# Kernel optimization log

Hardware: AMD Instinct MI355X
Metric: run time of the kernel (lower is better)

The kernel has to match this reference:

```python
import jax, jax.numpy as jnp
import numpy as np

B, N, C = 4, 1024, 23          # batch, nodes, scalar input channels (Rs_in=[(23,0)])
NB, H = 3, 100                 # cosine basis size, radial MLP hidden width
MAX_R = 3.0                    # CosineBasisModel max_radius
D1, D2, D3 = 30, 10, 1         # fc1/fc2/fc3 head dims


def setup_inputs() -> dict:
    key = jax.random.key(0)
    ks = jax.random.split(key, 12)
    features = jax.random.normal(ks[0], (B, N, C), jnp.float32)
    # random points inside a box comparable to max_radius so edges hit the basis support
    geometry = jax.random.uniform(ks[1], (B, N, 3), jnp.float32) * MAX_R
    # radial MLP (CosineBasisModel): NB -> H (relu) -> C weights (l=0 -> l=0 path, mul 23*1)
    W_rb1 = jax.random.normal(ks[2], (NB, H), jnp.float32) / np.sqrt(NB)
    b_rb1 = jnp.zeros((H,), jnp.float32)
    W_rb2 = jax.random.normal(ks[3], (H, C), jnp.float32) / np.sqrt(H)
    b_rb2 = jnp.zeros((C,), jnp.float32)
    # dense MLP head: Linear(N,30) -> Linear(30,10) -> Linear(10,1)
    W_fc1 = jax.random.normal(ks[4], (N, D1), jnp.float32) / np.sqrt(N)
    b_fc1 = jnp.zeros((D1,), jnp.float32)
    W_fc2 = jax.random.normal(ks[5], (D1, D2), jnp.float32) / np.sqrt(D1)
    b_fc2 = jnp.zeros((D2,), jnp.float32)
    W_fc3 = jax.random.normal(ks[6], (D2, D3), jnp.float32) / np.sqrt(D2)
    b_fc3 = jnp.zeros((D3,), jnp.float32)
    return {
        "features": features, "geometry": geometry,
        "W_rb1": W_rb1, "b_rb1": b_rb1, "W_rb2": W_rb2, "b_rb2": b_rb2,
        "W_fc1": W_fc1, "b_fc1": b_fc1, "W_fc2": W_fc2, "b_fc2": b_fc2,
        "W_fc3": W_fc3, "b_fc3": b_fc3,
    }


def _cosine_basis(r):
    """e3nn CosineBasisModel basis: cos^2 bumps centered on linspace(0,max_r,NB). r: [...]->[...,NB]."""
    radii = jnp.linspace(0.0, MAX_R, NB, dtype=r.dtype)
    step = radii[1] - radii[0]
    u = (r[..., None] - radii) / step
    half_pi = jnp.asarray(np.pi / 2, r.dtype)
    return jnp.where(jnp.abs(u) < 1.0, jnp.cos(half_pi * u) ** 2, jnp.zeros_like(u))


def reference(features, geometry, W_rb1, b_rb1, W_rb2, b_rb2,
              W_fc1, b_fc1, W_fc2, b_fc2, W_fc3, b_fc3):
    diff = geometry[:, :, None, :] - geometry[:, None, :, :]      # [B,N,N,3]
    r = jnp.sqrt(jnp.sum(diff * diff, axis=-1) + 1e-12)           # [B,N,N]
    basis = _cosine_basis(r)                                      # [B,N,N,NB]
    h = jax.nn.relu(basis @ W_rb1 + b_rb1)                        # [B,N,N,H]
    w = h @ W_rb2 + b_rb2                                         # [B,N,N,C] per-edge radial weights
    # scatter-sum weighted neighbor features -> scalar per node, 1/sqrt(N) kernel norm
    conv = jnp.einsum('zabc,zbc->za', w, features) / jnp.sqrt(jnp.asarray(N, w.dtype))  # [B,N]
    x = jax.nn.relu(conv @ W_fc1 + b_fc1)                         # [B,30]
    x = jax.nn.relu(x @ W_fc2 + b_fc2)                            # [B,10]
    x = x @ W_fc3 + b_fc3                                         # [B,1]
    return x
```

## Files before the change

### kernel.cpp

```cpp
#include <hip/hip_runtime.h>

#define Nn 1024
#define Cc 23
#define Hh 100
#define KN 128
#define DSTR 132
#define MUSCALE 28.2222222f
#define MUCLAMP 126.999f
#define NB 1024

#define UT_OFF     0
#define WF1T_OFF   4096
#define G4_OFF     34816
#define BIAS_OFF   51200
#define COLSUM_OFF 51204
#define PB_OFF     51264

__device__ __forceinline__ float rdlane(float v, int l) {
    return __int_as_float(__builtin_amdgcn_readlane(__float_as_int(v), l));
}

__global__ __launch_bounds__(256)
void prep_kernel(const float* __restrict__ f,
                 const float* __restrict__ geom,
                 const float* __restrict__ W1,
                 const float* __restrict__ b1,
                 const float* __restrict__ W2,
                 const float* __restrict__ b2,
                 const float* __restrict__ Wf1,
                 float* __restrict__ ws) {
    int blk = blockIdx.x;
    int t = threadIdx.x;
    if (blk < 128) {
        __shared__ float w2s[Hh * Cc];
        __shared__ float hv_s[Hh];
        int k = blk;
        for (int j = t; j < Hh * Cc; j += 256) w2s[j] = W2[j];
        if (t < Hh) {
            float v = (float)k * (3.0f / 127.0f);
            const float HPI = 1.57079632679f;
            float c0 = cosf(HPI * v);
            float c1 = cosf(HPI * (v - 1.0f));
            float c2 = cosf(HPI * (v - 2.0f));
            float s0 = (v < 1.0f) ? c0 * c0 : 0.0f;
            float s1 = (fabsf(v - 1.0f) < 1.0f) ? c1 * c1 : 0.0f;
            float s2 = (v > 1.0f && v < 3.0f) ? c2 * c2 : 0.0f;
            float pre = fmaf(s0, W1[t],
                         fmaf(s1, W1[Hh + t],
                          fmaf(s2, W1[2 * Hh + t], b1[t])));
            hv_s[t] = fmaxf(pre, 0.f);
        }
        __syncthreads();
        if (t < Cc) {
            float a0 = 0.f, a1 = 0.f;
            #pragma unroll 4
            for (int h = 0; h < Hh; h += 2) {
                a0 = fmaf(hv_s[h],     w2s[h * Cc + t],       a0);
                a1 = fmaf(hv_s[h + 1], w2s[(h + 1) * Cc + t], a1);
            }
            ws[UT_OFF + t * KN + k] = a0 + a1;
        }
    } else if (blk < 144) {
        int zb = (blk - 128) * 256 + t;
        const float* g = geom + zb * 3;
        reinterpret_cast<float4*>(ws + G4_OFF)[zb] =
            make_float4(g[0], g[1], g[2], 0.f);
    } else if (blk < 148) {
        __shared__ float red[256];
        int z = blk - 144;
        float s = 0.f;
        #pragma unroll
        for (int rr = 0; rr < 4; ++rr) {
            const float* fr = f + ((z << 10) + rr * 256 + t) * Cc;
            #pragma unroll
            for (int c = 0; c < Cc; ++c) s = fmaf(fr[c], b2[c], s);
        }
        red[t] = s; __syncthreads();
        for (int off = 128; off; off >>= 1) {
            if (t < off) red[t] += red[t + off];
            __syncthreads();
        }
        if (t == 0) ws[BIAS_OFF + z] = red[0];
    } else if (blk == 148) {
        __shared__ float cs_s[240];
        if (t < 240) {
            int d = t % 30, oct = t / 30;
            float c0 = 0.f, c1 = 0.f;
            #pragma unroll 4
            for (int j = 0; j < 128; j += 2) {
                c0 += Wf1[(oct * 128 + j) * 30 + d];
                c1 += Wf1[(oct * 128 + j + 1) * 30 + d];
            }
            cs_s[t] = c0 + c1;
        }
        __syncthreads();
        if (t < 30) {
            float cs = 0.f;
            #pragma unroll
            for (int o = 0; o < 8; ++o) cs += cs_s[o * 30 + t];
            ws[COLSUM_OFF + t] = cs;
        }
    } else {
        int d = blk - 149;
        #pragma unroll
        for (int j = 0; j < 4; ++j) {
            int k = j * 256 + t;
            ws[WF1T_OFF + d * Nn + k] = Wf1[k * 30 + d] * 0.03125f;
        }
    }
}

__global__ __launch_bounds__(256, 4)
void conv_kernel(const float* __restrict__ f,
                 const float* __restrict__ geom,
                 const float* __restrict__ ut,
                 const float4* __restrict__ geom4,
                 const float4* __restrict__ wf1t4,
                 float* __restrict__ pb) {
    __shared__ float lds_d[16 * DSTR];
    const int bid = blockIdx.x;
    const int t = threadIdx.x;
    const int lane = t & 63;
    const int wv = __builtin_amdgcn_readfirstlane(t >> 6);
    const int z = bid >> 8;
    const int aq = (bid >> 6) & 3;
    const int s = bid & 63;
    const int b0 = s * 16;
    const int k = t & 127;
    const int rh = __builtin_amdgcn_readfirstlane(t >> 7);

    float ur[Cc];
    #pragma unroll
    for (int c = 0; c < Cc; ++c) ur[c] = ut[c * KN + k];
    float fr[3];
    {
        int base = ((z << 10) + b0 + rh * 8) * Cc;
        #pragma unroll
        for (int j = 0; j < 3; ++j) {
            int off = j * 64 + lane;
            if (off > 183) off = 183;
            fr[j] = f[base + off];
        }
    }
    float gr;
    {
        int off = lane < 48 ? lane : 47;
        gr = geom[((z << 10) + b0) * 3 + off];
    }
    float4 ga = geom4[(z << 10) + (aq << 8) + t];

    #pragma unroll
    for (int r = 0; r < 8; ++r) {
        float a0 = 0.f, a1 = 0.f, a2 = 0.f, a3 = 0.f;
        #pragma unroll
        for (int c = 0; c < 20; c += 4) {
            a0 = fmaf(rdlane(fr[(r * Cc + c + 0) >> 6], (r * Cc + c + 0) & 63), ur[c + 0], a0);
            a1 = fmaf(rdlane(fr[(r * Cc + c + 1) >> 6], (r * Cc + c + 1) & 63), ur[c + 1], a1);
            a2 = fmaf(rdlane(fr[(r * Cc + c + 2) >> 6], (r * Cc + c + 2) & 63), ur[c + 2], a2);
            a3 = fmaf(rdlane(fr[(r * Cc + c + 3) >> 6], (r * Cc + c + 3) & 63), ur[c + 3], a3);
        }
        a0 = fmaf(rdlane(fr[(r * Cc + 20) >> 6], (r * Cc + 20) & 63), ur[20], a0);
        a1 = fmaf(rdlane(fr[(r * Cc + 21) >> 6], (r * Cc + 21) & 63), ur[21], a1);
        a2 = fmaf(rdlane(fr[(r * Cc + 22) >> 6], (r * Cc + 22) & 63), ur[22], a2);
        lds_d[(rh * 8 + r) * DSTR + k] = (a0 + a1) + (a2 + a3);
    }
    __syncthreads();

    float acc = 0.f;
    #pragma unroll
    for (int bl = 0; bl < 16; ++bl) {
        float dx = ga.x - rdlane(gr, bl * 3 + 0);
        float dy = ga.y - rdlane(gr, bl * 3 + 1);
        float dz = ga.z - rdlane(gr, bl * 3 + 2);
        float r = sqrtf(fmaf(dx, dx, fmaf(dy, dy, fmaf(dz, dz, 1e-12f))));
        float mu = fminf(r * MUSCALE, MUCLAMP);
        int m = (int)mu;
        float tt = mu - (float)m;
        const float* row = lds_d + bl * DSTR + m;
        float d0 = row[0];
        float d1 = row[1];
        acc += fmaf(tt, d1 - d0, d0);
    }
    __syncthreads();

    lds_d[t] = acc;
    __syncthreads();
    {
        const float4* a4 = reinterpret_cast<const float4*>(lds_d);
        float4 av = a4[lane];
        #pragma unroll
        for (int i = 0; i < 8; ++i) {
            int d = wv + 4 * i;
            if (d < 30) {
                float4 w = wf1t4[d * 256 + (aq << 6) + lane];
                float sum = av.x * w.x + av.y * w.y + av.z * w.z + av.w * w.w;
                #pragma unroll
                for (int off = 32; off; off >>= 1) sum += __shfl_down(sum, off);
                if (lane == 0) pb[d * NB + bid] = sum;
            }
        }
    }
}

__global__ __launch_bounds__(256)
void head_kernel(const float* __restrict__ ws,
                 const float* __restrict__ bf1,
                 const float* __restrict__ Wf2, const float* __restrict__ bf2,
                 const float* __restrict__ Wf3, const float* __restrict__ bf3,
                 float* __restrict__ out) {
    __shared__ float tail[448];
    int t = threadIdx.x;
    int p = t >> 1, half = t & 1;
    if (p < 120) {
        int zz = p / 30, d = p % 30;
        const float4* pbp = reinterpret_cast<const float4*>(
            ws + PB_OFF + d * NB + zz * 256 + half * 128);
        float s0 = 0.f, s1 = 0.f, s2 = 0.f, s3 = 0.f;
        #pragma unroll 8
        for (int j = 0; j < 32; ++j) {
            float4 v = pbp[j];
            s0 += v.x; s1 += v.y; s2 += v.z; s3 += v.w;
        }
        tail[t] = (s0 + s1) + (s2 + s3);
    }
    __syncthreads();
    if (t < 120) {
        int zz = t / 30, d = t % 30;
        float x1 = tail[2 * t] + tail[2 * t + 1]
                 + ws[BIAS_OFF + zz] * 0.03125f * ws[COLSUM_OFF + d]
                 + bf1[d];
        tail[256 + t] = fmaxf(x1, 0.f);
    }
    __syncthreads();
    if (t < 40) {
        int zz = t / 10, d = t % 10;
        float sm = bf2[d];
        #pragma unroll
        for (int kk = 0; kk < 30; ++kk)
            sm = fmaf(tail[256 + zz * 30 + kk], Wf2[kk * 10 + d], sm);
        tail[400 + t] = fmaxf(sm, 0.f);
    }
    __syncthreads();
    if (t < 4) {
        float sm = bf3[0];
        #pragma unroll
        for (int kk = 0; kk < 10; ++kk)
            sm = fmaf(tail[400 + t * 10 + kk], Wf3[kk], sm);
        out[t] = sm;
    }
}

extern "C" void kernel_launch(void* const* d_in, const int* in_sizes, int n_in,
                              void* d_out, int out_size, void* d_ws, size_t ws_size,
                              hipStream_t stream) {
    const float* f   = (const float*)d_in[0];
    const float* geo = (const float*)d_in[1];
    const float* W1  = (const float*)d_in[2];
    const float* b1  = (const float*)d_in[3];
    const float* W2  = (const float*)d_in[4];
    const float* b2  = (const float*)d_in[5];
    const float* Wf1 = (const float*)d_in[6];
    const float* bf1 = (const float*)d_in[7];
    const float* Wf2 = (const float*)d_in[8];
    const float* bf2 = (const float*)d_in[9];
    const float* Wf3 = (const float*)d_in[10];
    const float* bf3 = (const float*)d_in[11];
    float* ws  = (float*)d_ws;
    float* out = (float*)d_out;

    hipLaunchKernelGGL(prep_kernel, dim3(179), dim3(256), 0, stream,
                       f, geo, W1, b1, W2, b2, Wf1, ws);
    hipLaunchKernelGGL(conv_kernel, dim3(NB), dim3(256), 0, stream,
                       f, geo, ws + UT_OFF,
                       reinterpret_cast<const float4*>(ws + G4_OFF),
                       reinterpret_cast<const float4*>(ws + WF1T_OFF),
                       ws + PB_OFF);
    hipLaunchKernelGGL(head_kernel, dim3(1), dim3(256), 0, stream,
                       ws, bf1, Wf2, bf2, Wf3, bf3, out);
}
```

Before: 26.65 us.

## Split per-node D table into separate kernel and parallelize head reduction

The feature-by-radial-table product D is now computed once per node by a new kernel and written to global memory. Before, each of the four conv blocks sharing a node range recomputed it. The conv kernel now just copies its 16 D rows into LDS. The single-block head reduction is also split into a 30-block partial-sum kernel plus a small fc2/fc3 kernel. Together this adds two kernel launches and a global round-trip for D in exchange for less redundant FMA work and a more parallel reduction.

After: 26.10 us. 2.1% less time.

```diff
diff --git a/kernel.cpp b/kernel.cpp
--- a/kernel.cpp
+++ b/kernel.cpp
@@ -14,7 +14,9 @@
 #define G4_OFF     34816
 #define BIAS_OFF   51200
 #define COLSUM_OFF 51204
-#define PB_OFF     51264
+#define D_OFF      51264
+#define PB_OFF     575552
+#define X1PRE_OFF  606272
 
 __device__ __forceinline__ float rdlane(float v, int l) {
     return __int_as_float(__builtin_amdgcn_readlane(__float_as_int(v), l));
@@ -110,10 +112,49 @@
     }
 }
 
+__global__ __launch_bounds__(256)
+void dgemm_kernel(const float* __restrict__ f,
+                  const float* __restrict__ ut,
+                  float* __restrict__ D) {
+    const int bid = blockIdx.x;
+    const int t = threadIdx.x;
+    const int lane = t & 63;
+    const int k = t & 127;
+    const int rh = __builtin_amdgcn_readfirstlane(t >> 7);
+    float ur[Cc];
+    #pragma unroll
+    for (int c = 0; c < Cc; ++c) ur[c] = ut[c * KN + k];
+    const int row0 = bid * 8 + rh * 4;
+    float fr[2];
+    {
+        int base = row0 * Cc;
+        #pragma unroll
+        for (int j = 0; j < 2; ++j) {
+            int off = j * 64 + lane;
+            if (off > 91) off = 91;
+            fr[j] = f[base + off];
+        }
+    }
+    #pragma unroll
+    for (int r = 0; r < 4; ++r) {
+        float a0 = 0.f, a1 = 0.f, a2 = 0.f, a3 = 0.f;
+        #pragma unroll
+        for (int c = 0; c < 20; c += 4) {
+            a0 = fmaf(rdlane(fr[(r * Cc + c + 0) >> 6], (r * Cc + c + 0) & 63), ur[c + 0], a0);
+            a1 = fmaf(rdlane(fr[(r * Cc + c + 1) >> 6], (r * Cc + c + 1) & 63), ur[c + 1], a1);
+            a2 = fmaf(rdlane(fr[(r * Cc + c + 2) >> 6], (r * Cc + c + 2) & 63), ur[c + 2], a2);
+            a3 = fmaf(rdlane(fr[(r * Cc + c + 3) >> 6], (r * Cc + c + 3) & 63), ur[c + 3], a3);
+        }
+        a0 = fmaf(rdlane(fr[(r * Cc + 20) >> 6], (r * Cc + 20) & 63), ur[20], a0);
+        a1 = fmaf(rdlane(fr[(r * Cc + 21) >> 6], (r * Cc + 21) & 63), ur[21], a1);
+        a2 = fmaf(rdlane(fr[(r * Cc + 22) >> 6], (r * Cc + 22) & 63), ur[22], a2);
+        D[(row0 + r) * KN + k] = (a0 + a1) + (a2 + a3);
+    }
+}
+
 __global__ __launch_bounds__(256, 4)
-void conv_kernel(const float* __restrict__ f,
-                 const float* __restrict__ geom,
-                 const float* __restrict__ ut,
+void conv_kernel(const float* __restrict__ geom,
+                 const float* __restrict__ Dg,
                  const float4* __restrict__ geom4,
                  const float4* __restrict__ wf1t4,
                  float* __restrict__ pb) {
@@ -126,20 +167,13 @@
     const int aq = (bid >> 6) & 3;
     const int s = bid & 63;
     const int b0 = s * 16;
-    const int k = t & 127;
-    const int rh = __builtin_amdgcn_readfirstlane(t >> 7);
-
-    float ur[Cc];
-    #pragma unroll
-    for (int c = 0; c < Cc; ++c) ur[c] = ut[c * KN + k];
-    float fr[3];
+
     {
-        int base = ((z << 10) + b0 + rh * 8) * Cc;
-        #pragma unroll
-        for (int j = 0; j < 3; ++j) {
-            int off = j * 64 + lane;
-            if (off > 183) off = 183;
-            fr[j] = f[base + off];
+        const float4* src = reinterpret_cast<const float4*>(Dg + ((z << 10) + b0) * KN);
+        #pragma unroll
+        for (int j = t; j < 512; j += 256) {
+            int row = j >> 5, k4 = j & 31;
+            reinterpret_cast<float4*>(lds_d)[row * 33 + k4] = src[j];
         }
     }
     float gr;
@@ -148,22 +182,6 @@
         gr = geom[((z << 10) + b0) * 3 + off];
     }
     float4 ga = geom4[(z << 10) + (aq << 8) + t];
-
-    #pragma unroll
-    for (int r = 0; r < 8; ++r) {
-        float a0 = 0.f, a1 = 0.f, a2 = 0.f, a3 = 0.f;
-        #pragma unroll
-        for (int c = 0; c < 20; c += 4) {
-            a0 = fmaf(rdlane(fr[(r * Cc + c + 0) >> 6], (r * Cc + c + 0) & 63), ur[c + 0], a0);
-            a1 = fmaf(rdlane(fr[(r * Cc + c + 1) >> 6], (r * Cc + c + 1) & 63), ur[c + 1], a1);
-            a2 = fmaf(rdlane(fr[(r * Cc + c + 2) >> 6], (r * Cc + c + 2) & 63), ur[c + 2], a2);
-            a3 = fmaf(rdlane(fr[(r * Cc + c + 3) >> 6], (r * Cc + c + 3) & 63), ur[c + 3], a3);
-        }
-        a0 = fmaf(rdlane(fr[(r * Cc + 20) >> 6], (r * Cc + 20) & 63), ur[20], a0);
-        a1 = fmaf(rdlane(fr[(r * Cc + 21) >> 6], (r * Cc + 21) & 63), ur[21], a1);
-        a2 = fmaf(rdlane(fr[(r * Cc + 22) >> 6], (r * Cc + 22) & 63), ur[22], a2);
-        lds_d[(rh * 8 + r) * DSTR + k] = (a0 + a1) + (a2 + a3);
-    }
     __syncthreads();
 
     float acc = 0.f;
@@ -203,49 +221,49 @@
 }
 
 __global__ __launch_bounds__(256)
-void head_kernel(const float* __restrict__ ws,
+void head1_kernel(const float* __restrict__ pb,
+                  float* __restrict__ x1pre) {
+    int d = blockIdx.x;
+    int t = threadIdx.x;
+    const float4* p4 = reinterpret_cast<const float4*>(pb + d * NB);
+    float4 v = p4[t];
+    float s = (v.x + v.y) + (v.z + v.w);
+    #pragma unroll
+    for (int off = 32; off; off >>= 1) s += __shfl_down(s, off);
+    if ((t & 63) == 0) x1pre[d * 4 + (t >> 6)] = s;
+}
+
+__global__ __launch_bounds__(128)
+void fc23_kernel(const float* __restrict__ ws,
                  const float* __restrict__ bf1,
                  const float* __restrict__ Wf2, const float* __restrict__ bf2,
                  const float* __restrict__ Wf3, const float* __restrict__ bf3,
                  float* __restrict__ out) {
-    __shared__ float tail[448];
+    __shared__ float x1s[120];
+    __shared__ float x2s[40];
     int t = threadIdx.x;
-    int p = t >> 1, half = t & 1;
-    if (p < 120) {
-        int zz = p / 30, d = p % 30;
-        const float4* pbp = reinterpret_cast<const float4*>(
-            ws + PB_OFF + d * NB + zz * 256 + half * 128);
-        float s0 = 0.f, s1 = 0.f, s2 = 0.f, s3 = 0.f;
-        #pragma unroll 8
-        for (int j = 0; j < 32; ++j) {
-            float4 v = pbp[j];
-            s0 += v.x; s1 += v.y; s2 += v.z; s3 += v.w;
-        }
-        tail[t] = (s0 + s1) + (s2 + s3);
-    }
-    __syncthreads();
     if (t < 120) {
-        int zz = t / 30, d = t % 30;
-        float x1 = tail[2 * t] + tail[2 * t + 1]
-                 + ws[BIAS_OFF + zz] * 0.03125f * ws[COLSUM_OFF + d]
+        int z = t / 30, d = t % 30;
+        float x1 = ws[X1PRE_OFF + d * 4 + z]
+                 + ws[BIAS_OFF + z] * 0.03125f * ws[COLSUM_OFF + d]
                  + bf1[d];
-        tail[256 + t] = fmaxf(x1, 0.f);
+        x1s[t] = fmaxf(x1, 0.f);
     }
     __syncthreads();
     if (t < 40) {
-        int zz = t / 10, d = t % 10;
+        int z = t / 10, d = t % 10;
         float sm = bf2[d];
         #pragma unroll
         for (int kk = 0; kk < 30; ++kk)
-            sm = fmaf(tail[256 + zz * 30 + kk], Wf2[kk * 10 + d], sm);
-        tail[400 + t] = fmaxf(sm, 0.f);
+            sm = fmaf(x1s[z * 30 + kk], Wf2[kk * 10 + d], sm);
+        x2s[t] = fmaxf(sm, 0.f);
     }
     __syncthreads();
     if (t < 4) {
         float sm = bf3[0];
         #pragma unroll
         for (int kk = 0; kk < 10; ++kk)
-            sm = fmaf(tail[400 + t * 10 + kk], Wf3[kk], sm);
+            sm = fmaf(x2s[t * 10 + kk], Wf3[kk], sm);
         out[t] = sm;
     }
 }
@@ -270,11 +288,15 @@
 
     hipLaunchKernelGGL(prep_kernel, dim3(179), dim3(256), 0, stream,
                        f, geo, W1, b1, W2, b2, Wf1, ws);
+    hipLaunchKernelGGL(dgemm_kernel, dim3(512), dim3(256), 0, stream,
+                       f, ws + UT_OFF, ws + D_OFF);
     hipLaunchKernelGGL(conv_kernel, dim3(NB), dim3(256), 0, stream,
-                       f, geo, ws + UT_OFF,
+                       geo, ws + D_OFF,
                        reinterpret_cast<const float4*>(ws + G4_OFF),
                        reinterpret_cast<const float4*>(ws + WF1T_OFF),
                        ws + PB_OFF);
-    hipLaunchKernelGGL(head_kernel, dim3(1), dim3(256), 0, stream,
+    hipLaunchKernelGGL(head1_kernel, dim3(30), dim3(256), 0, stream,
+                       ws + PB_OFF, ws + X1PRE_OFF);
+    hipLaunchKernelGGL(fc23_kernel, dim3(1), dim3(128), 0, stream,
                        ws, bf1, Wf2, bf2, Wf3, bf3, out);
 }
```

## Fuse head into conv via atomics and last-block reduction, halve grid

Applied to the files above, without the earlier changes.

Merges the head kernel into the conv kernel. Each block atomically adds its fc1 partial sums into a small 120-entry buffer, and the last block to finish, detected with a global counter, runs the MLP head. The grid is also halved so each block processes two 256-node halves of the output nodes and reuses its per-block LDS table. This removes one kernel launch and the partial-sum buffer round trip, in exchange for atomic contention on 120 addresses, lower occupancy, and non-deterministic float summation order.

New measurement: 87.11 us. 227% more time.

```diff
diff --git a/kernel.cpp b/kernel.cpp
--- a/kernel.cpp
+++ b/kernel.cpp
@@ -7,14 +7,15 @@
 #define DSTR 132
 #define MUSCALE 28.2222222f
 #define MUCLAMP 126.999f
-#define NB 1024
+#define NBC 512
 
 #define UT_OFF     0
 #define WF1T_OFF   4096
 #define G4_OFF     34816
 #define BIAS_OFF   51200
 #define COLSUM_OFF 51204
-#define PB_OFF     51264
+#define X1PRE_OFF  51264
+#define CTR_OFF    51392
 
 __device__ __forceinline__ float rdlane(float v, int l) {
     return __int_as_float(__builtin_amdgcn_readlane(__float_as_int(v), l));
@@ -100,6 +101,8 @@
             for (int o = 0; o < 8; ++o) cs += cs_s[o * 30 + t];
             ws[COLSUM_OFF + t] = cs;
         }
+        if (t < 120) ws[X1PRE_OFF + t] = 0.f;
+        if (t == 120) reinterpret_cast<unsigned*>(ws + CTR_OFF)[0] = 0u;
     } else {
         int d = blk - 149;
         #pragma unroll
@@ -110,20 +113,25 @@
     }
 }
 
-__global__ __launch_bounds__(256, 4)
-void conv_kernel(const float* __restrict__ f,
-                 const float* __restrict__ geom,
-                 const float* __restrict__ ut,
-                 const float4* __restrict__ geom4,
-                 const float4* __restrict__ wf1t4,
-                 float* __restrict__ pb) {
+__global__ __launch_bounds__(256, 2)
+void megaconv_kernel(const float* __restrict__ f,
+                     const float* __restrict__ geom,
+                     const float* __restrict__ ut,
+                     const float4* __restrict__ geom4,
+                     const float4* __restrict__ wf1t4,
+                     float* __restrict__ ws,
+                     const float* __restrict__ bf1,
+                     const float* __restrict__ Wf2, const float* __restrict__ bf2,
+                     const float* __restrict__ Wf3, const float* __restrict__ bf3,
+                     float* __restrict__ out) {
     __shared__ float lds_d[16 * DSTR];
+    __shared__ int lastflag;
     const int bid = blockIdx.x;
     const int t = threadIdx.x;
     const int lane = t & 63;
     const int wv = __builtin_amdgcn_readfirstlane(t >> 6);
-    const int z = bid >> 8;
-    const int aq = (bid >> 6) & 3;
+    const int z = bid >> 7;
+    const int ah = (bid >> 6) & 1;
     const int s = bid & 63;
     const int b0 = s * 16;
     const int k = t & 127;
@@ -147,7 +155,8 @@
         int off = lane < 48 ? lane : 47;
         gr = geom[((z << 10) + b0) * 3 + off];
     }
-    float4 ga = geom4[(z << 10) + (aq << 8) + t];
+    float4 ga0 = geom4[(z << 10) + (ah << 9) + t];
+    float4 ga1 = geom4[(z << 10) + (ah << 9) + 256 + t];
 
     #pragma unroll
     for (int r = 0; r < 8; ++r) {
@@ -166,70 +175,76 @@
     }
     __syncthreads();
 
-    float acc = 0.f;
+    float acc0 = 0.f, acc1 = 0.f;
     #pragma unroll
     for (int bl = 0; bl < 16; ++bl) {
-        float dx = ga.x - rdlane(gr, bl * 3 + 0);
-        float dy = ga.y - rdlane(gr, bl * 3 + 1);
-        float dz = ga.z - rdlane(gr, bl * 3 + 2);
-        float r = sqrtf(fmaf(dx, dx, fmaf(dy, dy, fmaf(dz, dz, 1e-12f))));
-        float mu = fminf(r * MUSCALE, MUCLAMP);
-        int m = (int)mu;
-        float tt = mu - (float)m;
-        const float* row = lds_d + bl * DSTR + m;
-        float d0 = row[0];
-        float d1 = row[1];
-        acc += fmaf(tt, d1 - d0, d0);
-    }
-    __syncthreads();
-
-    lds_d[t] = acc;
+        float gbx = rdlane(gr, bl * 3 + 0);
+        float gby = rdlane(gr, bl * 3 + 1);
+        float gbz = rdlane(gr, bl * 3 + 2);
+        const float* row = lds_d + bl * DSTR;
+        {
+            float dx = ga0.x - gbx, dy = ga0.y - gby, dz = ga0.z - gbz;
+            float r = sqrtf(fmaf(dx, dx, fmaf(dy, dy, fmaf(dz, dz, 1e-12f))));
+            float mu = fminf(r * MUSCALE, MUCLAMP);
+            int m = (int)mu;
+            float tt = mu - (float)m;
+            float d0 = row[m];
+            float d1 = row[m + 1];
+            acc0 += fmaf(tt, d1 - d0, d0);
+        }
+        {
+            float dx = ga1.x - gbx, dy = ga1.y - gby, dz = ga1.z - gbz;
+            float r = sqrtf(fmaf(dx, dx, fmaf(dy, dy, fmaf(dz, dz, 1e-12f))));
+            float mu = fminf(r * MUSCALE, MUCLAMP);
+            int m = (int)mu;
+            float tt = mu - (float)m;
+            float d0 = row[m];
+            float d1 = row[m + 1];
+            acc1 += fmaf(tt, d1 - d0, d0);
+        }
+    }
+    __syncthreads();
+
+    lds_d[t] = acc0;
+    lds_d[256 + t] = acc1;
     __syncthreads();
     {
         const float4* a4 = reinterpret_cast<const float4*>(lds_d);
-        float4 av = a4[lane];
+        float4 av0 = a4[lane];
+        float4 av1 = a4[64 + lane];
         #pragma unroll
         for (int i = 0; i < 8; ++i) {
             int d = wv + 4 * i;
             if (d < 30) {
-                float4 w = wf1t4[d * 256 + (aq << 6) + lane];
-                float sum = av.x * w.x + av.y * w.y + av.z * w.z + av.w * w.w;
+                float4 w0 = wf1t4[d * 256 + (ah << 7) + lane];
+                float4 w1 = wf1t4[d * 256 + (ah << 7) + 64 + lane];
+                float sum = av0.x * w0.x + av0.y * w0.y + av0.z * w0.z + av0.w * w0.w
+                          + av1.x * w1.x + av1.y * w1.y + av1.z * w1.z + av1.w * w1.w;
                 #pragma unroll
                 for (int off = 32; off; off >>= 1) sum += __shfl_down(sum, off);
-                if (lane == 0) pb[d * NB + bid] = sum;
+                if (lane == 0) atomicAdd(&ws[X1PRE_OFF + d * 4 + z], sum);
             }
         }
     }
-}
-
-__global__ __launch_bounds__(256)
-void head_kernel(const float* __restrict__ ws,
-                 const float* __restrict__ bf1,
-                 const float* __restrict__ Wf2, const float* __restrict__ bf2,
-                 const float* __restrict__ Wf3, const float* __restrict__ bf3,
-                 float* __restrict__ out) {
-    __shared__ float tail[448];
-    int t = threadIdx.x;
-    int p = t >> 1, half = t & 1;
-    if (p < 120) {
-        int zz = p / 30, d = p % 30;
-        const float4* pbp = reinterpret_cast<const float4*>(
-            ws + PB_OFF + d * NB + zz * 256 + half * 128);
-        float s0 = 0.f, s1 = 0.f, s2 = 0.f, s3 = 0.f;
-        #pragma unroll 8
-        for (int j = 0; j < 32; ++j) {
-            float4 v = pbp[j];
-            s0 += v.x; s1 += v.y; s2 += v.z; s3 += v.w;
-        }
-        tail[t] = (s0 + s1) + (s2 + s3);
-    }
-    __syncthreads();
+
+    __syncthreads();
+    if (t == 0) {
+        unsigned* ctr = reinterpret_cast<unsigned*>(ws + CTR_OFF);
+        unsigned r = __hip_atomic_fetch_add(ctr, 1u, __ATOMIC_ACQ_REL,
+                                            __HIP_MEMORY_SCOPE_AGENT);
+        lastflag = (r == NBC - 1) ? 1 : 0;
+    }
+    __syncthreads();
+    if (!lastflag) return;
+
+    float* x1s = lds_d;
+    float* x2s = lds_d + 128;
     if (t < 120) {
-        int zz = t / 30, d = t % 30;
-        float x1 = tail[2 * t] + tail[2 * t + 1]
+        int zz = t & 3, d = t >> 2;
+        float x1 = ws[X1PRE_OFF + t]
                  + ws[BIAS_OFF + zz] * 0.03125f * ws[COLSUM_OFF + d]
                  + bf1[d];
-        tail[256 + t] = fmaxf(x1, 0.f);
+        x1s[zz * 30 + d] = fmaxf(x1, 0.f);
     }
     __syncthreads();
     if (t < 40) {
@@ -237,15 +252,15 @@
         float sm = bf2[d];
         #pragma unroll
         for (int kk = 0; kk < 30; ++kk)
-            sm = fmaf(tail[256 + zz * 30 + kk], Wf2[kk * 10 + d], sm);
-        tail[400 + t] = fmaxf(sm, 0.f);
+            sm = fmaf(x1s[zz * 30 + kk], Wf2[kk * 10 + d], sm);
+        x2s[t] = fmaxf(sm, 0.f);
     }
     __syncthreads();
     if (t < 4) {
         float sm = bf3[0];
         #pragma unroll
         for (int kk = 0; kk < 10; ++kk)
-            sm = fmaf(tail[400 + t * 10 + kk], Wf3[kk], sm);
+            sm = fmaf(x2s[t * 10 + kk], Wf3[kk], sm);
         out[t] = sm;
     }
 }
@@ -270,11 +285,9 @@
 
     hipLaunchKernelGGL(prep_kernel, dim3(179), dim3(256), 0, stream,
                        f, geo, W1, b1, W2, b2, Wf1, ws);
-    hipLaunchKernelGGL(conv_kernel, dim3(NB), dim3(256), 0, stream,
+    hipLaunchKernelGGL(megaconv_kernel, dim3(NBC), dim3(256), 0, stream,
                        f, geo, ws + UT_OFF,
                        reinterpret_cast<const float4*>(ws + G4_OFF),
                        reinterpret_cast<const float4*>(ws + WF1T_OFF),
-                       ws + PB_OFF);
-    hipLaunchKernelGGL(head_kernel, dim3(1), dim3(256), 0, stream,
                        ws, bf1, Wf2, bf2, Wf3, bf3, out);
 }
```
